# Kernel tuning notes

Hardware: AMD Instinct MI355X
Metric: run time of the kernel (lower is better)

## Reference

```python
import jax, jax.numpy as jnp
import numpy as np

B, CIN, COUT = 4, 32, 32
D1, D2, D3 = 64, 64, 64
M1, M2, M3 = 32, 32, 17  # n_modes with last dim -> 32//2+1 after rfft redundancy
INIT_STD = (2.0 / (CIN + COUT)) ** 0.5


def setup_inputs() -> dict:
    key = jax.random.key(0)
    k_x, k_wr, k_wi, k_b = jax.random.split(key, 4)
    x = jax.random.normal(k_x, (B, CIN, D1, D2, D3), dtype=jnp.float32)
    # ComplexDense factorized weight, normal_(0, init_std) on real and imag parts
    w_real = INIT_STD * jax.random.normal(k_wr, (CIN, COUT, M1, M2, M3), dtype=jnp.float32)
    w_imag = INIT_STD * jax.random.normal(k_wi, (CIN, COUT, M1, M2, M3), dtype=jnp.float32)
    # bias: (n_layers=1, out_channels, 1, 1, 1); we take index 0 slice
    bias = INIT_STD * jax.random.normal(k_b, (1, COUT, 1, 1, 1), dtype=jnp.float32)
    return {"x": x, "w_real": w_real, "w_imag": w_imag, "bias": bias}


def reference(x, w_real, w_imag, bias):
    fft_axes = (-3, -2, -1)
    b, cin, d1, d2, d3 = x.shape
    f3 = d3 // 2 + 1
    # forward rFFT, shift all but last (real) axis so low modes are centered
    xf = jnp.fft.rfftn(x, axes=fft_axes)               # (B, Cin, D1, D2, f3) complex
    xf = jnp.fft.fftshift(xf, axes=fft_axes[:-1])
    weight = w_real + 1j * w_imag                       # (Cin, Cout, M1, M2, M3)
    m1, m2, m3 = weight.shape[2:]
    s1, s2 = (d1 - m1) // 2, (d2 - m2) // 2
    xs = xf[:, :, s1:s1 + m1, s2:s2 + m2, :m3]          # centered low modes
    # channel contraction in Fourier space: abcde,bfcde->afcde
    out_modes = jnp.einsum('abcde,bfcde->afcde', xs, weight)
    out_fft = jnp.zeros((b, weight.shape[1], d1, d2, f3), dtype=out_modes.dtype)
    out_fft = out_fft.at[:, :, s1:s1 + m1, s2:s2 + m2, :m3].set(out_modes)
    # torch applies fftshift (not ifftshift); identical for even sizes
    out_fft = jnp.fft.fftshift(out_fft, axes=fft_axes[:-1])
    out = jnp.fft.irfftn(out_fft, s=(d1, d2, d3), axes=fft_axes)
    return out + bias[0]
```

## Files before the change

kernel.cpp:

```cpp
#include <hip/hip_runtime.h>
#include <math.h>

static constexpr int NB  = 4;
static constexpr int NC  = 32;

__device__ __attribute__((aligned(256))) float T3F[64 * 48];
__device__ __attribute__((aligned(256))) float2 T3I2[17 * 64];
__device__ __attribute__((aligned(256))) float T12F[64 * 64];
__device__ __attribute__((aligned(256))) float TINV[32 * 128];

__global__ __launch_bounds__(256) void k0_init() {
    const int t = blockIdx.x * 256 + threadIdx.x;
    if (t < 64 * 17) {
        int n = t / 17, k = t % 17;
        int idx = (n * k) & 63;
        float s, c;
        sincospif(idx / 32.0f, &s, &c);
        T3F[n * 48 + 2 * k] = c;  T3F[n * 48 + 2 * k + 1] = -s;
    }
    if (t < 64) {
        for (int q = 34; q < 48; ++q) T3F[t * 48 + q] = 0.f;
    }
    if (t < 17 * 64) {
        int k = t >> 6, n = t & 63;
        int idx = (n * k) & 63;
        float s, c;
        sincospif(idx / 32.0f, &s, &c);
        T3I2[t] = make_float2(c, s);
    }
    if (t < 64 * 32) {
        int n = t / 32, p = t % 32;
        int o = (p + 48) & 63;
        int idx = (o * n) & 63;
        float s, c;
        sincospif(idx / 32.0f, &s, &c);
        T12F[n * 64 + 2 * p] = c;  T12F[n * 64 + 2 * p + 1] = -s;
    }
    if (t < 32 * 64) {
        int p = t / 64, n = t % 64;
        int o = (p + 48) & 63;
        int idx = (o * n) & 63;
        float s, c;
        sincospif(idx / 32.0f, &s, &c);
        TINV[p * 128 + 2 * n] = c;  TINV[p * 128 + 2 * n + 1] = s;
    }
}

__device__ __forceinline__ void cmadd(float2& a, float2 x, float wx, float wy) {
    a.x = fmaf(x.x, wx, fmaf(-x.y, wy, a.x));
    a.y = fmaf(x.x, wy, fmaf( x.y, wx, a.y));
}

__global__ __launch_bounds__(64)
void k1_rfft_d3(const float* __restrict__ x, float2* __restrict__ o1) {
    __shared__ float tile[64 * 65];
    const int t = threadIdx.x, bid = blockIdx.x;
    const float4* src4 = (const float4*)(x + (size_t)bid * 4096);
    for (int j = 0; j < 16; ++j) {
        int f4 = j * 64 + t;
        float4 v = src4[f4];
        int d2 = f4 >> 4, n0 = (f4 & 15) << 2;
        float* p = &tile[d2 * 65 + n0];
        p[0] = v.x; p[1] = v.y; p[2] = v.z; p[3] = v.w;
    }
    __syncthreads();
    float ar[17], ai[17];
#pragma unroll
    for (int k = 0; k < 17; ++k) { ar[k] = 0.f; ai[k] = 0.f; }
    const float* row = &tile[t * 65];
    for (int n = 0; n < 64; ++n) {
        float xv = row[n];
        const float* w = &T3F[n * 48];
#pragma unroll
        for (int k = 0; k < 17; ++k) {
            ar[k] = fmaf(xv, w[2 * k], ar[k]);
            ai[k] = fmaf(xv, w[2 * k + 1], ai[k]);
        }
    }
    const int bc = bid >> 6, d1 = bid & 63;
    float2* dst = o1 + (size_t)bc * (17 * 4096) + d1 * 64 + t;
#pragma unroll
    for (int k = 0; k < 17; ++k)
        dst[(size_t)k * 4096] = make_float2(ar[k], ai[k]);
}

__global__ __launch_bounds__(256)
void k2a_dft_d2(const float2* __restrict__ in, float2* __restrict__ T) {
    __shared__ float smem[8320];
    float* re = smem;
    float* im = smem + 64 * 65;
    const int t = threadIdx.x;
    const size_t base = (size_t)blockIdx.x * 4096;
    for (int j = 0; j < 16; ++j) {
        int idx = j * 256 + t;
        float2 v = in[base + idx];
        int d1 = idx >> 6, n2 = idx & 63;
        re[d1 * 65 + n2] = v.x;
        im[d1 * 65 + n2] = v.y;
    }
    __syncthreads();
    const int d1 = t & 63;
    const int pg = __builtin_amdgcn_readfirstlane(t >> 6);
    float2 acc[8];
#pragma unroll
    for (int j = 0; j < 8; ++j) acc[j] = make_float2(0.f, 0.f);
    const float* rrow = &re[d1 * 65];
    const float* irow = &im[d1 * 65];
#pragma unroll 2
    for (int n2 = 0; n2 < 64; ++n2) {
        float xr = rrow[n2], xi = irow[n2];
        const float* w = &T12F[n2 * 64 + pg * 16];
#pragma unroll
        for (int j = 0; j < 8; ++j)
            cmadd(acc[j], make_float2(xr, xi), w[2 * j], w[2 * j + 1]);
    }
    __syncthreads();
    float2* tile = (float2*)smem;
#pragma unroll
    for (int j = 0; j < 8; ++j) tile[d1 * 33 + pg * 8 + j] = acc[j];
    __syncthreads();
    float2* dst = T + (size_t)blockIdx.x * 2048;
#pragma unroll
    for (int q = 0; q < 8; ++q) {
        int e = t * 8 + q;
        dst[e] = tile[(e >> 5) * 33 + (e & 31)];
    }
}

__global__ __launch_bounds__(544)
void k2b_dft_d1(const float2* __restrict__ T, float2* __restrict__ Y) {
    __shared__ float2 tile[8 * 544];
    const int u = threadIdx.x;
    const int bc = blockIdx.x, pg = blockIdx.y;
    const int k3 = u >> 5, p2 = u & 31;
    const float2* src = T + ((size_t)bc * 17 + k3) * 2048 + p2;
    float2 acc[8];
#pragma unroll
    for (int j = 0; j < 8; ++j) acc[j] = make_float2(0.f, 0.f);
#pragma unroll 2
    for (int n1 = 0; n1 < 64; ++n1) {
        float2 xv = src[n1 * 32];
        const float* w = &T12F[n1 * 64 + pg * 16];
#pragma unroll
        for (int j = 0; j < 8; ++j)
            cmadd(acc[j], xv, w[2 * j], w[2 * j + 1]);
    }
#pragma unroll
    for (int j = 0; j < 8; ++j)
        tile[j * 544 + p2 * 17 + k3] = acc[j];
    __syncthreads();
    float2* dst = Y + (size_t)bc * 17408 + (size_t)pg * 8 * 544;
#pragma unroll
    for (int i = 0; i < 8; ++i)
        dst[u + i * 544] = tile[u + i * 544];
}

__global__ __launch_bounds__(64)
void k3_mix(const float2* __restrict__ Y, const float* __restrict__ wr,
            const float* __restrict__ wi, float2* __restrict__ Z) {
    const int m = blockIdx.x * 64 + threadIdx.x;
    const int ch = blockIdx.y;
    float2 acc[4][4];
#pragma unroll
    for (int a = 0; a < 4; ++a)
#pragma unroll
        for (int co = 0; co < 4; ++co) acc[a][co] = make_float2(0.f, 0.f);
#pragma unroll 8
    for (int cin = 0; cin < 32; ++cin) {
        float2 xv[4];
#pragma unroll
        for (int a = 0; a < 4; ++a)
            xv[a] = Y[((size_t)a * 32 + cin) * 17408 + m];
        size_t wb = ((size_t)cin * 32 + ch * 4) * 17408 + m;
#pragma unroll
        for (int co = 0; co < 4; ++co) {
            float wrv = wr[wb + (size_t)co * 17408];
            float wiv = wi[wb + (size_t)co * 17408];
#pragma unroll
            for (int a = 0; a < 4; ++a)
                cmadd(acc[a][co], xv[a], wrv, wiv);
        }
    }
#pragma unroll
    for (int a = 0; a < 4; ++a)
#pragma unroll
        for (int co = 0; co < 4; ++co)
            Z[((size_t)a * 32 + ch * 4 + co) * 17408 + m] = acc[a][co];
}

__global__ __launch_bounds__(544)
void k4a_idft_d1(const float2* __restrict__ Z, float2* __restrict__ U) {
    const int u = threadIdx.x;
    const int bf = blockIdx.x, ng = blockIdx.y;
    const float2* src = Z + (size_t)bf * 17408 + u;
    float2 acc[8];
#pragma unroll
    for (int j = 0; j < 8; ++j) acc[j] = make_float2(0.f, 0.f);
#pragma unroll 2
    for (int p1 = 0; p1 < 32; ++p1) {
        float2 xv = src[(size_t)p1 * 544];
        const float* w = &TINV[p1 * 128 + ng * 16];
#pragma unroll
        for (int j = 0; j < 8; ++j)
            cmadd(acc[j], xv, w[2 * j], w[2 * j + 1]);
    }
    float2* dst = U + (size_t)bf * 34816 + (size_t)ng * 8 * 544 + u;
#pragma unroll
    for (int j = 0; j < 8; ++j) dst[(size_t)j * 544] = acc[j];
}

__global__ __launch_bounds__(256)
void k45_ifft23(const float2* __restrict__ U, const float* __restrict__ bias,
                float* __restrict__ out) {
    __shared__ __align__(16) float2 Ur[32 * 18];
    __shared__ float2 W2[17 * 64];
    const int t = threadIdx.x;
    const int bf = blockIdx.x, n1 = blockIdx.y;
    const float2* src = U + (size_t)bf * 34816 + (size_t)n1 * 544;
    for (int j = t; j < 544; j += 256) {
        int p2 = j / 17, k3 = j - p2 * 17;
        Ur[p2 * 18 + k3] = src[j];
    }
    const int lane = t & 63;
    const int w = __builtin_amdgcn_readfirstlane(t >> 6);
    float2 tws[32];
#pragma unroll
    for (int p = 0; p < 32; ++p)
        tws[p] = *(const float2*)&TINV[p * 128 + 2 * lane];
    __syncthreads();
    const float inv2 = 2.0f / 262144.0f;
    {
        const int kb = w * 4;
        float A[4] = {0,0,0,0}, Bm[4] = {0,0,0,0};
        float C[4] = {0,0,0,0}, Dm[4] = {0,0,0,0};
#pragma unroll
        for (int p2 = 0; p2 < 32; ++p2) {
            float4 xa = *(const float4*)&Ur[p2 * 18 + kb];
            float4 xb = *(const float4*)&Ur[p2 * 18 + kb + 2];
            float c = tws[p2].x, s = tws[p2].y;
            A[0] = fmaf(xa.x, c, A[0]);  Bm[0] = fmaf(xa.y, s, Bm[0]);
            C[0] = fmaf(xa.x, s, C[0]);  Dm[0] = fmaf(xa.y, c, Dm[0]);
            A[1] = fmaf(xa.z, c, A[1]);  Bm[1] = fmaf(xa.w, s, Bm[1]);
            C[1] = fmaf(xa.z, s, C[1]);  Dm[1] = fmaf(xa.w, c, Dm[1]);
            A[2] = fmaf(xb.x, c, A[2]);  Bm[2] = fmaf(xb.y, s, Bm[2]);
            C[2] = fmaf(xb.x, s, C[2]);  Dm[2] = fmaf(xb.y, c, Dm[2]);
            A[3] = fmaf(xb.z, c, A[3]);  Bm[3] = fmaf(xb.w, s, Bm[3]);
            C[3] = fmaf(xb.z, s, C[3]);  Dm[3] = fmaf(xb.w, c, Dm[3]);
        }
#pragma unroll
        for (int j = 0; j < 4; ++j)
            W2[(kb + j) * 64 + lane] =
                make_float2((A[j] - Bm[j]) * inv2, (C[j] + Dm[j]) * inv2);
        if (w == 3) {
            float a = 0.f, b = 0.f, c2 = 0.f, d = 0.f;
#pragma unroll
            for (int p2 = 0; p2 < 32; ++p2) {
                float2 xv = Ur[p2 * 18 + 16];
                float c = tws[p2].x, s = tws[p2].y;
                a  = fmaf(xv.x, c, a);   b = fmaf(xv.y, s, b);
                c2 = fmaf(xv.x, s, c2);  d = fmaf(xv.y, c, d);
            }
            W2[16 * 64 + lane] = make_float2((a - b) * inv2, (c2 + d) * inv2);
        }
    }
    __syncthreads();
    float2 X[17];
#pragma unroll
    for (int k = 0; k < 17; ++k) X[k] = W2[k * 64 + lane];
    const float bv = bias[bf & 31];
    float y[16];
#pragma unroll
    for (int r = 0; r < 16; ++r) y[r] = fmaf(X[0].x, 0.5f, bv);
#pragma unroll
    for (int k = 1; k < 17; ++k) {
        const float2* tr = &T3I2[k * 64 + w * 16];
#pragma unroll
        for (int r = 0; r < 16; ++r) {
            float2 tw = tr[r];
            y[r] = fmaf(X[k].x, tw.x, y[r]);
            y[r] = fmaf(-X[k].y, tw.y, y[r]);
        }
    }
    float* dst = out + (size_t)bf * 262144 + (size_t)n1 * 4096
               + (size_t)lane * 64 + w * 16;
#pragma unroll
    for (int q = 0; q < 4; ++q)
        *(float4*)&dst[q * 4] =
            make_float4(y[q * 4], y[q * 4 + 1], y[q * 4 + 2], y[q * 4 + 3]);
}

extern "C" void kernel_launch(void* const* d_in, const int* in_sizes, int n_in,
                              void* d_out, int out_size, void* d_ws, size_t ws_size,
                              hipStream_t stream) {
    const float* x    = (const float*)d_in[0];
    const float* wr   = (const float*)d_in[1];
    const float* wi   = (const float*)d_in[2];
    const float* bias = (const float*)d_in[3];
    float* out = (float*)d_out;

    float2* A = (float2*)d_ws;
    float2* B = A + (size_t)2176 * 4096;
    float2* Y = A;
    float2* Z = A + (size_t)17825792 / 8;

    k0_init    <<<8, 256, 0, stream>>>();
    k1_rfft_d3 <<<NB * NC * 64, 64, 0, stream>>>(x, A);
    k2a_dft_d2 <<<2176, 256, 0, stream>>>(A, B);
    k2b_dft_d1 <<<dim3(128, 4), 544, 0, stream>>>(B, Y);
    k3_mix     <<<dim3(272, 8), 64, 0, stream>>>(Y, wr, wi, Z);
    k4a_idft_d1<<<dim3(128, 8), 544, 0, stream>>>(Z, B);
    k45_ifft23 <<<dim3(128, 64), 256, 0, stream>>>(B, bias, out);
}
```

Before: 293.3 us.

## Give each wavefront its own n1 row in final inverse FFT kernel

The final inverse transform kernel now assigns one n1 plane per wavefront, four per block, instead of one plane per 256-thread block. Each wavefront loads its own slice into private LDS, computes all 17 d2-stage outputs in registers, and then writes a whole row of 64 d3 outputs. This removes both block-wide barriers and the shared W2 staging buffer, and cuts the block count by four. In exchange each thread does more serial work and holds more registers (X[17] plus 32 twiddles), which may limit occupancy; the writes become per-lane strided float4 stores across a 256-byte row.

```diff
diff --git a/kernel.cpp b/kernel.cpp
--- a/kernel.cpp
+++ b/kernel.cpp
@@ -209,84 +209,74 @@
     for (int j = 0; j < 8; ++j) dst[(size_t)j * 544] = acc[j];
 }
 
-__global__ __launch_bounds__(256)
-void k45_ifft23(const float2* __restrict__ U, const float* __restrict__ bias,
-                float* __restrict__ out) {
-    __shared__ __align__(16) float2 Ur[32 * 18];
-    __shared__ float2 W2[17 * 64];
+__global__ __launch_bounds__(256, 4)
+void k45w_ifft23(const float2* __restrict__ U, const float* __restrict__ bias,
+                 float* __restrict__ out) {
+    __shared__ __align__(16) float2 Ur[4][576];
     const int t = threadIdx.x;
-    const int bf = blockIdx.x, n1 = blockIdx.y;
-    const float2* src = U + (size_t)bf * 34816 + (size_t)n1 * 544;
-    for (int j = t; j < 544; j += 256) {
-        int p2 = j / 17, k3 = j - p2 * 17;
-        Ur[p2 * 18 + k3] = src[j];
-    }
     const int lane = t & 63;
     const int w = __builtin_amdgcn_readfirstlane(t >> 6);
+    const int bf = blockIdx.x;
+    const int n1 = blockIdx.y * 4 + w;
+    float2* ur = Ur[w];
     float2 tws[32];
 #pragma unroll
     for (int p = 0; p < 32; ++p)
         tws[p] = *(const float2*)&TINV[p * 128 + 2 * lane];
-    __syncthreads();
+    const float2* src = U + (size_t)bf * 34816 + (size_t)n1 * 544;
+    {
+        int j = lane;
+#pragma unroll
+        for (int it = 0; it < 8; ++it) {
+            float2 v = src[j];
+            ur[(j / 17) * 18 + (j % 17)] = v;
+            j += 64;
+        }
+        if (lane < 32) {
+            int jj = 512 + lane;
+            float2 v = src[jj];
+            ur[(jj / 17) * 18 + (jj % 17)] = v;
+        }
+    }
+    float2 X[17];
+#pragma unroll
+    for (int k = 0; k < 17; ++k) X[k] = make_float2(0.f, 0.f);
+#pragma unroll
+    for (int p2 = 0; p2 < 32; ++p2) {
+        const float2* up = &ur[p2 * 18];
+        const float c = tws[p2].x, s = tws[p2].y;
+#pragma unroll
+        for (int h = 0; h < 8; ++h) {
+            float4 q = *(const float4*)&up[h * 2];
+            X[2 * h].x     = fmaf(q.x, c, fmaf(-q.y, s, X[2 * h].x));
+            X[2 * h].y     = fmaf(q.x, s, fmaf( q.y, c, X[2 * h].y));
+            X[2 * h + 1].x = fmaf(q.z, c, fmaf(-q.w, s, X[2 * h + 1].x));
+            X[2 * h + 1].y = fmaf(q.z, s, fmaf( q.w, c, X[2 * h + 1].y));
+        }
+        float2 qt = up[16];
+        X[16].x = fmaf(qt.x, c, fmaf(-qt.y, s, X[16].x));
+        X[16].y = fmaf(qt.x, s, fmaf( qt.y, c, X[16].y));
+    }
     const float inv2 = 2.0f / 262144.0f;
-    {
-        const int kb = w * 4;
-        float A[4] = {0,0,0,0}, Bm[4] = {0,0,0,0};
-        float C[4] = {0,0,0,0}, Dm[4] = {0,0,0,0};
-#pragma unroll
-        for (int p2 = 0; p2 < 32; ++p2) {
-            float4 xa = *(const float4*)&Ur[p2 * 18 + kb];
-            float4 xb = *(const float4*)&Ur[p2 * 18 + kb + 2];
-            float c = tws[p2].x, s = tws[p2].y;
-            A[0] = fmaf(xa.x, c, A[0]);  Bm[0] = fmaf(xa.y, s, Bm[0]);
-            C[0] = fmaf(xa.x, s, C[0]);  Dm[0] = fmaf(xa.y, c, Dm[0]);
-            A[1] = fmaf(xa.z, c, A[1]);  Bm[1] = fmaf(xa.w, s, Bm[1]);
-            C[1] = fmaf(xa.z, s, C[1]);  Dm[1] = fmaf(xa.w, c, Dm[1]);
-            A[2] = fmaf(xb.x, c, A[2]);  Bm[2] = fmaf(xb.y, s, Bm[2]);
-            C[2] = fmaf(xb.x, s, C[2]);  Dm[2] = fmaf(xb.y, c, Dm[2]);
-            A[3] = fmaf(xb.z, c, A[3]);  Bm[3] = fmaf(xb.w, s, Bm[3]);
-            C[3] = fmaf(xb.z, s, C[3]);  Dm[3] = fmaf(xb.w, c, Dm[3]);
-        }
-#pragma unroll
-        for (int j = 0; j < 4; ++j)
-            W2[(kb + j) * 64 + lane] =
-                make_float2((A[j] - Bm[j]) * inv2, (C[j] + Dm[j]) * inv2);
-        if (w == 3) {
-            float a = 0.f, b = 0.f, c2 = 0.f, d = 0.f;
-#pragma unroll
-            for (int p2 = 0; p2 < 32; ++p2) {
-                float2 xv = Ur[p2 * 18 + 16];
-                float c = tws[p2].x, s = tws[p2].y;
-                a  = fmaf(xv.x, c, a);   b = fmaf(xv.y, s, b);
-                c2 = fmaf(xv.x, s, c2);  d = fmaf(xv.y, c, d);
-            }
-            W2[16 * 64 + lane] = make_float2((a - b) * inv2, (c2 + d) * inv2);
-        }
-    }
-    __syncthreads();
-    float2 X[17];
-#pragma unroll
-    for (int k = 0; k < 17; ++k) X[k] = W2[k * 64 + lane];
+#pragma unroll
+    for (int k = 0; k < 17; ++k) { X[k].x *= inv2; X[k].y *= inv2; }
     const float bv = bias[bf & 31];
-    float y[16];
-#pragma unroll
-    for (int r = 0; r < 16; ++r) y[r] = fmaf(X[0].x, 0.5f, bv);
-#pragma unroll
-    for (int k = 1; k < 17; ++k) {
-        const float2* tr = &T3I2[k * 64 + w * 16];
-#pragma unroll
-        for (int r = 0; r < 16; ++r) {
-            float2 tw = tr[r];
-            y[r] = fmaf(X[k].x, tw.x, y[r]);
-            y[r] = fmaf(-X[k].y, tw.y, y[r]);
-        }
-    }
-    float* dst = out + (size_t)bf * 262144 + (size_t)n1 * 4096
-               + (size_t)lane * 64 + w * 16;
-#pragma unroll
-    for (int q = 0; q < 4; ++q)
-        *(float4*)&dst[q * 4] =
-            make_float4(y[q * 4], y[q * 4 + 1], y[q * 4 + 2], y[q * 4 + 3]);
+    float* dst = out + (size_t)bf * 262144 + (size_t)n1 * 4096 + (size_t)lane * 64;
+#pragma unroll
+    for (int nq = 0; nq < 16; ++nq) {
+        float y0 = fmaf(X[0].x, 0.5f, bv);
+        float y1 = y0, y2 = y0, y3 = y0;
+#pragma unroll
+        for (int k = 1; k < 17; ++k) {
+            const float2* tr = &T3I2[k * 64 + nq * 4];
+            float2 t0 = tr[0], t1 = tr[1], t2 = tr[2], t3 = tr[3];
+            y0 = fmaf(X[k].x, t0.x, y0);  y0 = fmaf(-X[k].y, t0.y, y0);
+            y1 = fmaf(X[k].x, t1.x, y1);  y1 = fmaf(-X[k].y, t1.y, y1);
+            y2 = fmaf(X[k].x, t2.x, y2);  y2 = fmaf(-X[k].y, t2.y, y2);
+            y3 = fmaf(X[k].x, t3.x, y3);  y3 = fmaf(-X[k].y, t3.y, y3);
+        }
+        *(float4*)&dst[nq * 4] = make_float4(y0, y1, y2, y3);
+    }
 }
 
 extern "C" void kernel_launch(void* const* d_in, const int* in_sizes, int n_in,
@@ -309,5 +299,5 @@
     k2b_dft_d1 <<<dim3(128, 4), 544, 0, stream>>>(B, Y);
     k3_mix     <<<dim3(272, 8), 64, 0, stream>>>(Y, wr, wi, Z);
     k4a_idft_d1<<<dim3(128, 8), 544, 0, stream>>>(Z, B);
-    k45_ifft23 <<<dim3(128, 64), 256, 0, stream>>>(B, bias, out);
-}
+    k45w_ifft23<<<dim3(128, 16), 256, 0, stream>>>(B, bias, out);
+}
```

After: 303.3 us. 3.4% more time.
